# Optimization experiments

Hardware: AMD Instinct MI355X
Metric: run time of the kernel (lower is better)

Reference implementation:

```python
import jax, jax.numpy as jnp
import numpy as np

B, T, C, H = 16, 4096, 256, 256

def setup_inputs() -> dict:
    key = jax.random.key(0)
    kx, kwi, kbi, kwh, kbh = jax.random.split(key, 5)
    s = 1.0 / np.sqrt(C)
    return {
        "x": jax.random.normal(kx, (B, T, C), dtype=jnp.float32),
        "Wi": jax.random.uniform(kwi, (H, C), dtype=jnp.float32, minval=-s, maxval=s),
        "bi": jax.random.uniform(kbi, (H,), dtype=jnp.float32, minval=-s, maxval=s),
        "Wh": jax.random.uniform(kwh, (H, H), dtype=jnp.float32, minval=-s, maxval=s),
        "bh": jax.random.uniform(kbh, (H,), dtype=jnp.float32, minval=-s, maxval=s),
    }

def reference(x, Wi, bi, Wh, bh):
    # Faithful to the source: Cell computes tanh(i2h(x) + h2h(x)) -- both
    # linears applied to x_t, the hidden state is never consumed, so there
    # is no recurrence and all timesteps can be computed in one fused pass.
    # hidden_states: [B, T, H]
    hidden_states = jnp.tanh(
        jnp.einsum("btc,hc->bth", x, Wi) + bi
        + jnp.einsum("btc,hc->bth", x, Wh) + bh
    )
    h_last = hidden_states[:, -1, :]  # h after the loop
    return (hidden_states, h_last)
```

## Files before the change

kernel.cpp:

```cpp
#include <hip/hip_runtime.h>


using short8 = __attribute__((ext_vector_type(8))) short;
using f32x4  = __attribute__((ext_vector_type(4))) float;

constexpr int Tn = 4096, Cn = 256, Hn = 256;
constexpr int Mn = 16 * Tn;

__device__ inline unsigned pack2_bf16(float a, float b) {
  unsigned ua = __float_as_uint(a);
  unsigned ub = __float_as_uint(b);
  ua += 0x7fffu + ((ua >> 16) & 1u);
  ub += 0x7fffu + ((ub >> 16) & 1u);
  return (ua >> 16) | (ub & 0xffff0000u);
}

union u4s8 { uint4 u; short8 s; };

__global__ __launch_bounds__(512, 4) void fused_gemm_tanh(
    const float* __restrict__ x, const float* __restrict__ Wi,
    const float* __restrict__ bi, const float* __restrict__ Wh,
    const float* __restrict__ bh, float* __restrict__ out) {
  __shared__ __align__(16) unsigned short Bsm[128 * 256];

  const int tid   = threadIdx.x;
  const int mb    = blockIdx.x >> 1;
  const int nb    = blockIdx.x & 1;
  const int mBase = mb * 256;
  const int nBase = nb * 128;

#pragma unroll
  for (int i = 0; i < 8; i++) {
    int h = i * 512 + tid;
    int r = h >> 5;
    int c = h & 31;
    const float4* wi4 = (const float4*)(Wi + (size_t)(nBase + r) * Cn + c * 8);
    const float4* wh4 = (const float4*)(Wh + (size_t)(nBase + r) * Cn + c * 8);
    float4 a0 = wi4[0], a1 = wi4[1];
    float4 b0 = wh4[0], b1 = wh4[1];
    uint4 p;
    p.x = pack2_bf16(a0.x + b0.x, a0.y + b0.y);
    p.y = pack2_bf16(a0.z + b0.z, a0.w + b0.w);
    p.z = pack2_bf16(a1.x + b1.x, a1.y + b1.y);
    p.w = pack2_bf16(a1.z + b1.z, a1.w + b1.w);
    int pc = c ^ (r & 7);
    *(uint4*)&Bsm[(r << 8) + (pc << 3)] = p;
  }
  __syncthreads();

  const int wave = tid >> 6;
  const int lane = tid & 63;
  const int rid  = lane & 15;
  const int kgrp = lane >> 4;
  const int rowBase = mBase + wave * 32;

  f32x4 acc[2][8];
#pragma unroll
  for (int im = 0; im < 2; im++)
#pragma unroll
    for (int in = 0; in < 8; in++) acc[im][in] = (f32x4)0.f;

  const float* a0p = x + (size_t)(rowBase + rid) * Cn + kgrp * 8;
  const float* a1p = a0p + (size_t)16 * Cn;

#pragma unroll 2
  for (int kc = 0; kc < 8; kc++) {
    short8 af[2];
    {
      const float4* p0 = (const float4*)(a0p + kc * 32);
      const float4* p1 = (const float4*)(a1p + kc * 32);
      float4 v0 = p0[0], v1 = p0[1];
      float4 w0 = p1[0], w1 = p1[1];
      u4s8 t0, t1;
      t0.u.x = pack2_bf16(v0.x, v0.y); t0.u.y = pack2_bf16(v0.z, v0.w);
      t0.u.z = pack2_bf16(v1.x, v1.y); t0.u.w = pack2_bf16(v1.z, v1.w);
      t1.u.x = pack2_bf16(w0.x, w0.y); t1.u.y = pack2_bf16(w0.z, w0.w);
      t1.u.z = pack2_bf16(w1.x, w1.y); t1.u.w = pack2_bf16(w1.z, w1.w);
      af[0] = t0.s; af[1] = t1.s;
    }
    short8 bf[8];
    const int cbase = (kc << 2) | kgrp;
#pragma unroll
    for (int in = 0; in < 8; in++) {
      int ln = in * 16 + rid;
      bf[in] = *(const short8*)&Bsm[(ln << 8) + ((cbase ^ (ln & 7)) << 3)];
    }
#pragma unroll
    for (int im = 0; im < 2; im++)
#pragma unroll
      for (int in = 0; in < 8; in++)
        acc[im][in] = __builtin_amdgcn_mfma_f32_16x16x32_bf16(
            af[im], bf[in], acc[im][in], 0, 0, 0);
  }

#pragma unroll
  for (int in = 0; in < 8; in++) {
    int n = nBase + in * 16 + rid;
    float bias = bi[n] + bh[n];
#pragma unroll
    for (int im = 0; im < 2; im++) {
      int mrow = rowBase + im * 16 + kgrp * 4;
#pragma unroll
      for (int r = 0; r < 4; r++) {
        int m = mrow + r;
        float v = acc[im][in][r] + bias;
        float t = 1.f - 2.f / (__expf(2.f * v) + 1.f);
        out[(size_t)m * Hn + n] = t;
        if ((m & (Tn - 1)) == (Tn - 1))
          out[(size_t)Mn * Hn + (size_t)(m >> 12) * Hn + n] = t;
      }
    }
  }
}

extern "C" void kernel_launch(void* const* d_in, const int* in_sizes, int n_in,
                              void* d_out, int out_size, void* d_ws,
                              size_t ws_size, hipStream_t stream) {
  (void)in_sizes; (void)n_in; (void)out_size; (void)d_ws; (void)ws_size;
  const float* x  = (const float*)d_in[0];
  const float* Wi = (const float*)d_in[1];
  const float* bi = (const float*)d_in[2];
  const float* Wh = (const float*)d_in[3];
  const float* bh = (const float*)d_in[4];
  float* out = (float*)d_out;

  fused_gemm_tanh<<<512, 512, 0, stream>>>(x, Wi, bi, Wh, bh, out);
}
```

Measured before the change: 142.9 us.

## Precompute combined bf16 weights in prep kernel and prefetch x before LDS fill

Adds a prep kernel that sums Wi+Wh and bh+bi once into a bf16 workspace, so each GEMM block copies bf16 weights instead of re-reading and converting two fp32 matrices. The GEMM kernel now uses 256-thread blocks over 128x128 tiles, giving 1024 blocks. It issues all x loads for its rows into registers before the weight copy to overlap latency, and writes the output with nontemporal stores. The costs are an extra kernel launch, higher register pressure from the 32 float4 prefetch buffer, and twice as many blocks each staging weights into LDS.

```diff
diff --git a/kernel.cpp b/kernel.cpp
--- a/kernel.cpp
+++ b/kernel.cpp
@@ -17,36 +17,29 @@
 
 union u4s8 { uint4 u; short8 s; };
 
-__global__ __launch_bounds__(512, 4) void fused_gemm_tanh(
-    const float* __restrict__ x, const float* __restrict__ Wi,
-    const float* __restrict__ bi, const float* __restrict__ Wh,
-    const float* __restrict__ bh, float* __restrict__ out) {
+__global__ __launch_bounds__(256) void prep_kernel(
+    const float* __restrict__ Wi, const float* __restrict__ bi,
+    const float* __restrict__ Wh, const float* __restrict__ bh,
+    unsigned short* __restrict__ Wc, float* __restrict__ bc) {
+  int idx = blockIdx.x * 256 + threadIdx.x;
+  float w = Wi[idx] + Wh[idx];
+  unsigned u = __float_as_uint(w);
+  u += 0x7fffu + ((u >> 16) & 1u);
+  Wc[idx] = (unsigned short)(u >> 16);
+  if (blockIdx.x == 0) bc[threadIdx.x] = bi[threadIdx.x] + bh[threadIdx.x];
+}
+
+__global__ __launch_bounds__(256, 2) void gemm_tanh_kernel(
+    const float* __restrict__ x, const unsigned short* __restrict__ Wc,
+    const float* __restrict__ bc, float* __restrict__ out) {
   __shared__ __align__(16) unsigned short Bsm[128 * 256];
 
   const int tid   = threadIdx.x;
-  const int mb    = blockIdx.x >> 1;
-  const int nb    = blockIdx.x & 1;
-  const int mBase = mb * 256;
+  const int bid   = blockIdx.x;
+  const int mb    = bid & 511;
+  const int nb    = bid >> 9;
+  const int mBase = mb * 128;
   const int nBase = nb * 128;
-
-#pragma unroll
-  for (int i = 0; i < 8; i++) {
-    int h = i * 512 + tid;
-    int r = h >> 5;
-    int c = h & 31;
-    const float4* wi4 = (const float4*)(Wi + (size_t)(nBase + r) * Cn + c * 8);
-    const float4* wh4 = (const float4*)(Wh + (size_t)(nBase + r) * Cn + c * 8);
-    float4 a0 = wi4[0], a1 = wi4[1];
-    float4 b0 = wh4[0], b1 = wh4[1];
-    uint4 p;
-    p.x = pack2_bf16(a0.x + b0.x, a0.y + b0.y);
-    p.y = pack2_bf16(a0.z + b0.z, a0.w + b0.w);
-    p.z = pack2_bf16(a1.x + b1.x, a1.y + b1.y);
-    p.w = pack2_bf16(a1.z + b1.z, a1.w + b1.w);
-    int pc = c ^ (r & 7);
-    *(uint4*)&Bsm[(r << 8) + (pc << 3)] = p;
-  }
-  __syncthreads();
 
   const int wave = tid >> 6;
   const int lane = tid & 63;
@@ -54,30 +47,49 @@
   const int kgrp = lane >> 4;
   const int rowBase = mBase + wave * 32;
 
+  const float* a0p = x + (size_t)(rowBase + rid) * Cn + kgrp * 8;
+  const float* a1p = a0p + (size_t)16 * Cn;
+  float4 abuf[8][4];
+#pragma unroll
+  for (int kc = 0; kc < 8; kc++) {
+    const float4* p0 = (const float4*)(a0p + kc * 32);
+    const float4* p1 = (const float4*)(a1p + kc * 32);
+    abuf[kc][0] = p0[0];
+    abuf[kc][1] = p0[1];
+    abuf[kc][2] = p1[0];
+    abuf[kc][3] = p1[1];
+  }
+
+#pragma unroll
+  for (int i = 0; i < 16; i++) {
+    int h = i * 256 + tid;
+    int r = h >> 5;
+    int c = h & 31;
+    uint4 v = *(const uint4*)(Wc + (size_t)(nBase + r) * Cn + c * 8);
+    int pc = c ^ (r & 7);
+    *(uint4*)&Bsm[(r << 8) + (pc << 3)] = v;
+  }
+  __syncthreads();
+
   f32x4 acc[2][8];
 #pragma unroll
   for (int im = 0; im < 2; im++)
 #pragma unroll
     for (int in = 0; in < 8; in++) acc[im][in] = (f32x4)0.f;
 
-  const float* a0p = x + (size_t)(rowBase + rid) * Cn + kgrp * 8;
-  const float* a1p = a0p + (size_t)16 * Cn;
+#pragma unroll
+  for (int kc = 0; kc < 8; kc++) {
+    u4s8 t0, t1;
+    t0.u.x = pack2_bf16(abuf[kc][0].x, abuf[kc][0].y);
+    t0.u.y = pack2_bf16(abuf[kc][0].z, abuf[kc][0].w);
+    t0.u.z = pack2_bf16(abuf[kc][1].x, abuf[kc][1].y);
+    t0.u.w = pack2_bf16(abuf[kc][1].z, abuf[kc][1].w);
+    t1.u.x = pack2_bf16(abuf[kc][2].x, abuf[kc][2].y);
+    t1.u.y = pack2_bf16(abuf[kc][2].z, abuf[kc][2].w);
+    t1.u.z = pack2_bf16(abuf[kc][3].x, abuf[kc][3].y);
+    t1.u.w = pack2_bf16(abuf[kc][3].z, abuf[kc][3].w);
+    short8 af[2] = {t0.s, t1.s};
 
-#pragma unroll 2
-  for (int kc = 0; kc < 8; kc++) {
-    short8 af[2];
-    {
-      const float4* p0 = (const float4*)(a0p + kc * 32);
-      const float4* p1 = (const float4*)(a1p + kc * 32);
-      float4 v0 = p0[0], v1 = p0[1];
-      float4 w0 = p1[0], w1 = p1[1];
-      u4s8 t0, t1;
-      t0.u.x = pack2_bf16(v0.x, v0.y); t0.u.y = pack2_bf16(v0.z, v0.w);
-      t0.u.z = pack2_bf16(v1.x, v1.y); t0.u.w = pack2_bf16(v1.z, v1.w);
-      t1.u.x = pack2_bf16(w0.x, w0.y); t1.u.y = pack2_bf16(w0.z, w0.w);
-      t1.u.z = pack2_bf16(w1.x, w1.y); t1.u.w = pack2_bf16(w1.z, w1.w);
-      af[0] = t0.s; af[1] = t1.s;
-    }
     short8 bf[8];
     const int cbase = (kc << 2) | kgrp;
 #pragma unroll
@@ -96,7 +108,7 @@
 #pragma unroll
   for (int in = 0; in < 8; in++) {
     int n = nBase + in * 16 + rid;
-    float bias = bi[n] + bh[n];
+    float bias = bc[n];
 #pragma unroll
     for (int im = 0; im < 2; im++) {
       int mrow = rowBase + im * 16 + kgrp * 4;
@@ -105,7 +117,7 @@
         int m = mrow + r;
         float v = acc[im][in][r] + bias;
         float t = 1.f - 2.f / (__expf(2.f * v) + 1.f);
-        out[(size_t)m * Hn + n] = t;
+        __builtin_nontemporal_store(t, &out[(size_t)m * Hn + n]);
         if ((m & (Tn - 1)) == (Tn - 1))
           out[(size_t)Mn * Hn + (size_t)(m >> 12) * Hn + n] = t;
       }
@@ -116,7 +128,7 @@
 extern "C" void kernel_launch(void* const* d_in, const int* in_sizes, int n_in,
                               void* d_out, int out_size, void* d_ws,
                               size_t ws_size, hipStream_t stream) {
-  (void)in_sizes; (void)n_in; (void)out_size; (void)d_ws; (void)ws_size;
+  (void)in_sizes; (void)n_in; (void)out_size; (void)ws_size;
   const float* x  = (const float*)d_in[0];
   const float* Wi = (const float*)d_in[1];
   const float* bi = (const float*)d_in[2];
@@ -124,5 +136,9 @@
   const float* bh = (const float*)d_in[4];
   float* out = (float*)d_out;
 
-  fused_gemm_tanh<<<512, 512, 0, stream>>>(x, Wi, bi, Wh, bh, out);
+  unsigned short* Wc = (unsigned short*)d_ws;
+  float* bc = (float*)((char*)d_ws + (size_t)Hn * Cn * sizeof(unsigned short));
+
+  prep_kernel<<<(Hn * Cn) / 256, 256, 0, stream>>>(Wi, bi, Wh, bh, Wc, bc);
+  gemm_tanh_kernel<<<1024, 256, 0, stream>>>(x, Wc, bc, out);
 }
```

After: 135.9 us. -5.0%, faster.
